# Optimization experiments

Measured on AMD Instinct MI355X. Metric: run time of the kernel, lower is better.

The kernel has to match this reference:

```python
import jax, jax.numpy as jnp
import numpy as np
import math

PHI = (1 + math.sqrt(5)) / 2
PI = math.pi
B, L, D, V, NL, PAD = 2, 384, 256, 32000, 3, 0


def _ln(t, eps):
    mu = t.mean(-1, keepdims=True)
    var = ((t - mu) ** 2).mean(-1, keepdims=True)
    return (t - mu) / jnp.sqrt(var + eps)


def setup_inputs() -> dict:
    key = jax.random.key(0)
    ks = jax.random.split(key, 8)
    return {
        'x': jax.random.randint(ks[0], (B, L), 0, V, dtype=jnp.int32),
        'emb_real': jax.random.normal(ks[1], (V, D), jnp.float32) * 0.02,
        'emb_imag': jax.random.normal(ks[2], (V, D), jnp.float32) * 0.02,
        'layer_phases': jax.random.normal(ks[3], (NL, D), jnp.float32) * 0.02,
        'interference_weights': jax.random.normal(ks[4], (NL, D), jnp.float32) * 0.02,
        'energy_levels': jnp.linspace(0.0, 1.0, D).astype(jnp.float32),
        'excitation_factor': jnp.ones((1,), jnp.float32) * 0.1,
        'phase_preservation': jnp.ones((NL, D), jnp.float32) * 0.1,
        'coherence_factor': jnp.ones((NL, 1), jnp.float32) * 0.1,
        'W_attn': jax.random.normal(ks[5], (NL, D, D), jnp.float32) * 0.02,
        'out_w': jax.random.normal(ks[6], (2 * D, V), jnp.float32) * 0.02,
        'out_b': jnp.zeros((V,), jnp.float32),
    }


def _forward(x, emb_real, emb_imag, layer_phases, interference_weights,
             energy_levels, excitation_factor, phase_preservation,
             coherence_factor, W_attn, out_w, out_b):
    re = emb_real[x] * 0.1                      # [B,L,D]
    _unused_imag = emb_imag[x] * 0.1            # imag embedding unused downstream (as in original)
    # ---- EnhancedDynamicPhaseSpace ----
    fr = jnp.zeros_like(re)
    fi = jnp.zeros_like(re)
    for i in range(NL):
        pa = jnp.tanh(layer_phases[i]) * PI * PHI      # [D]
        r = _ln(re * jnp.cos(pa), 1e-8)
        im = _ln(re * jnp.sin(pa), 1e-8)
        w = jnp.tanh(interference_weights[i])
        r = r * w
        im = im * w
        a = 2.0 * PI * i / NL
        ca, sa = math.cos(a), math.sin(a)
        fr = fr + r * ca - im * sa
        fi = fi + r * sa + im * ca
    amp = jnp.sqrt(fr * fr + fi * fi + 1e-8)
    coll = (amp < 0.1).astype(re.dtype)
    exc = jnp.exp(energy_levels) * excitation_factor   # [D]
    fr = fr + coll * exc
    fi = fi + coll * exc
    nrm = jnp.sqrt(fr * fr + fi * fi + 1e-8)
    real = jnp.clip(fr / nrm, -1.0, 1.0)
    imag = jnp.clip(fi / nrm, -1.0, 1.0)
    # ---- 3 QuantumStatePreservingAttention layers ----
    pad_mask = (x == PAD)                               # [B,L]
    scale = D ** (-0.5)
    for i in range(NL):
        # q/k/v LayerNorms are parameter-free here and q=k=v, so one norm each
        nr = _ln(real, 1e-5)
        ni = _ln(imag, 1e-5)
        ph = jnp.arctan2(ni + 1e-8, nr + 1e-8)          # [B,L,D]
        pdiff = ph[:, :, None, :] - ph[:, None, :, :]   # [B,L,L,D]
        interf = jnp.cos(pdiff)                         # [B,L,L,D]
        # mean over last dim of (interf @ W) == interf . row-means of W (same math)
        w_mean = W_attn[i].mean(axis=1)                 # [D]
        scores = jnp.einsum('blmd,d->blm', interf, w_mean) * scale
        scores = jnp.where(pad_mask[:, None, :], -jnp.inf, scores)
        attn = jnp.clip(jax.nn.softmax(scores, axis=-1), 1e-6, 1.0)
        out_r = jnp.einsum('blm,bmd->bld', attn, nr)
        out_i = jnp.einsum('blm,bmd->bld', attn, ni)
        coh = interf.mean(axis=(-1, -2))                # [B,L]
        cf = jax.nn.sigmoid(coherence_factor[i]) * coh[..., None]
        phase = jnp.arctan2(out_i + 1e-8, out_r + 1e-8)
        pres = jax.nn.sigmoid(phase_preservation[i]) * cf
        pr = out_r * jnp.cos(phase * pres)
        pim = out_i * jnp.sin(phase * pres)
        real = jnp.clip(_ln(real + 0.01 * pr, 1e-8), -1.0, 1.0)
        _dead = _ln(imag + 0.01 * pim, 1e-8)            # computed then overwritten in original
        imag = real                                     # original bug: imag = clamp(real, -1, 1)
    combined = _ln(jnp.concatenate([real, imag], axis=-1), 1e-5)
    logits = jnp.clip((combined @ out_w + out_b) * 0.1, -10.0, 10.0)
    return logits


def reference(x, emb_real, emb_imag, layer_phases, interference_weights,
              energy_levels, excitation_factor, phase_preservation,
              coherence_factor, W_attn, out_w, out_b):
    return _forward(x, emb_real, emb_imag, layer_phases, interference_weights,
                    energy_levels, excitation_factor, phase_preservation,
                    coherence_factor, W_attn, out_w, out_b)
```

## Files before the change

kernel.cpp:

```cpp
#include <hip/hip_runtime.h>
#include <hip/hip_bf16.h>
#include <math.h>

typedef __hip_bfloat16 bf16;
typedef __bf16 bf16x8 __attribute__((ext_vector_type(8)));
typedef float f32x4 __attribute__((ext_vector_type(4)));

#define NTOK 768
#define SEQ  384
#define DDIM 256
#define VOC  32000

__device__ __forceinline__ float bf2f(bf16 v) { return __bfloat162float(v); }

__device__ __forceinline__ bool probe_bf(const void* energy) {
    return ((const unsigned short*)energy)[1] != 0;
}
__device__ __forceinline__ float ldin(const void* p, long i, bool bf) {
    return bf ? bf2f(((const bf16*)p)[i]) : ((const float*)p)[i];
}

__device__ __forceinline__ float blk_sum256(float v, float* red) {
    #pragma unroll
    for (int o = 32; o > 0; o >>= 1) v += __shfl_down(v, o, 64);
    int w = threadIdx.x >> 6;
    __syncthreads();
    if ((threadIdx.x & 63) == 0) red[w] = v;
    __syncthreads();
    return red[0] + red[1] + red[2] + red[3];
}

__global__ __launch_bounds__(256)
void phase_kernel(const int* __restrict__ x, const void* __restrict__ emb,
                  const void* __restrict__ lph, const void* __restrict__ iw,
                  const void* __restrict__ energy, const void* __restrict__ excf,
                  float* __restrict__ realO, float* __restrict__ imagO)
{
    __shared__ float red[4];
    bool bf = probe_bf(energy);
    int t = blockIdx.x, d = threadIdx.x;
    int tok = x[t];
    float re = ldin(emb, (long)tok * DDIM + d, bf) * 0.1f;
    float fr = 0.f, fi = 0.f;
    const float ca[3] = {1.0f, -0.5f, -0.5f};
    const float sa[3] = {0.0f, 0.86602540378443864676f, -0.86602540378443864676f};
    #pragma unroll
    for (int i = 0; i < 3; ++i) {
        float pa = tanhf(ldin(lph, i * DDIM + d, bf)) * 3.14159265358979323846f;
        pa = pa * 1.61803398874989484820f;
        float vr = re * cosf(pa);
        float vi = re * sinf(pa);
        float mu = blk_sum256(vr, red) * (1.f / 256.f);
        float dv = vr - mu;
        float var = blk_sum256(dv * dv, red) * (1.f / 256.f);
        float r = dv / sqrtf(var + 1e-8f);
        mu = blk_sum256(vi, red) * (1.f / 256.f);
        float di = vi - mu;
        var = blk_sum256(di * di, red) * (1.f / 256.f);
        float im = di / sqrtf(var + 1e-8f);
        float w = tanhf(ldin(iw, i * DDIM + d, bf));
        r *= w; im *= w;
        fr = fr + r * ca[i] - im * sa[i];
        fi = fi + r * sa[i] + im * ca[i];
    }
    float amp = sqrtf(fr * fr + fi * fi + 1e-8f);
    float ex = expf(ldin(energy, d, bf)) * ldin(excf, 0, bf);
    if (amp < 0.1f) { fr += ex; fi += ex; }
    float nrm = sqrtf(fr * fr + fi * fi + 1e-8f);
    float rr = fminf(fmaxf(fr / nrm, -1.f), 1.f);
    float ii = fminf(fmaxf(fi / nrm, -1.f), 1.f);
    realO[t * DDIM + d] = rr;
    imagO[t * DDIM + d] = ii;
}

__global__ __launch_bounds__(256)
void wmean_kernel(const void* __restrict__ W, const void* __restrict__ energy,
                  float* __restrict__ wmAll)
{
    bool bf = probe_bf(energy);
    int row = blockIdx.x * 4 + (threadIdx.x >> 6);
    int lane = threadIdx.x & 63;
    long base = (long)row * DDIM + lane * 4;
    float s = 0.f;
    #pragma unroll
    for (int j = 0; j < 4; ++j) s += ldin(W, base + j, bf);
    #pragma unroll
    for (int o = 32; o > 0; o >>= 1) s += __shfl_down(s, o, 64);
    if (lane == 0) wmAll[row] = s * (1.f / 256.f) * 0.0625f;
}

__global__ __launch_bounds__(256)
void normphase_kernel(const float* __restrict__ realI, const float* __restrict__ imagI,
                      const float* __restrict__ wm,
                      float* __restrict__ nrO, float* __restrict__ niO,
                      float* __restrict__ Co, float* __restrict__ So,
                      bf16* __restrict__ ASh, bf16* __restrict__ ASl,
                      bf16* __restrict__ BSh, bf16* __restrict__ BSl)
{
    __shared__ float red[4];
    int t = blockIdx.x, d = threadIdx.x;
    float r = realI[t * DDIM + d];
    float mu = blk_sum256(r, red) * (1.f / 256.f);
    float dv = r - mu;
    float var = blk_sum256(dv * dv, red) * (1.f / 256.f);
    float nr = dv / sqrtf(var + 1e-5f);
    float im = imagI[t * DDIM + d];
    mu = blk_sum256(im, red) * (1.f / 256.f);
    float di = im - mu;
    var = blk_sum256(di * di, red) * (1.f / 256.f);
    float ni = di / sqrtf(var + 1e-5f);
    float ph = atan2f(ni + 1e-8f, nr + 1e-8f);
    float Cv = cosf(ph), Sv = sinf(ph);
    nrO[t * DDIM + d] = nr;
    niO[t * DDIM + d] = ni;
    Co[t * DDIM + d] = Cv;
    So[t * DDIM + d] = Sv;
    float wv = wm[d];
    float aC = Cv * wv, aS = Sv * wv;
    long o0 = (long)t * 512 + d, o1 = o0 + 256;
    bf16 h;
    h = __float2bfloat16(aC); ASh[o0] = h; ASl[o0] = __float2bfloat16(aC - bf2f(h));
    h = __float2bfloat16(aS); ASh[o1] = h; ASl[o1] = __float2bfloat16(aS - bf2f(h));
    h = __float2bfloat16(Cv); BSh[o0] = h; BSl[o0] = __float2bfloat16(Cv - bf2f(h));
    h = __float2bfloat16(Sv); BSh[o1] = h; BSl[o1] = __float2bfloat16(Sv - bf2f(h));
}

__global__ __launch_bounds__(256)
void sums_kernel(const float* __restrict__ C, const float* __restrict__ S,
                 float* __restrict__ Cp, float* __restrict__ Sp)
{
    int c = blockIdx.x, b = blockIdx.y, d = threadIdx.x;
    float cs = 0.f, ss = 0.f;
    int base = (b * SEQ + c * 48) * DDIM + d;
    for (int m = 0; m < 48; ++m) { cs += C[base + m * DDIM]; ss += S[base + m * DDIM]; }
    Cp[(b * 8 + c) * DDIM + d] = cs;
    Sp[(b * 8 + c) * DDIM + d] = ss;
}

__global__ __launch_bounds__(256)
void transpose_kernel(const float* __restrict__ nr, const float* __restrict__ ni,
                      bf16* __restrict__ nrTh, bf16* __restrict__ nrTl,
                      bf16* __restrict__ niTh, bf16* __restrict__ niTl)
{
    __shared__ float tr[64][65], ti[64][65];
    int m0 = blockIdx.x * 64, d0 = blockIdx.y * 64, b = blockIdx.z;
    int c = threadIdx.x & 63, rr = threadIdx.x >> 6;
    #pragma unroll
    for (int i = 0; i < 16; ++i) {
        int r = i * 4 + rr;
        tr[r][c] = nr[(b * SEQ + m0 + r) * DDIM + d0 + c];
        ti[r][c] = ni[(b * SEQ + m0 + r) * DDIM + d0 + c];
    }
    __syncthreads();
    #pragma unroll
    for (int i = 0; i < 16; ++i) {
        int dd = i * 4 + rr;
        float vr = tr[c][dd], vi = ti[c][dd];
        long o = (long)(b * DDIM + d0 + dd) * SEQ + m0 + c;
        bf16 h;
        h = __float2bfloat16(vr); nrTh[o] = h; nrTl[o] = __float2bfloat16(vr - bf2f(h));
        h = __float2bfloat16(vi); niTh[o] = h; niTl[o] = __float2bfloat16(vi - bf2f(h));
    }
}

__device__ __forceinline__ void gload_lds16(const bf16* g, bf16* l) {
    __builtin_amdgcn_global_load_lds(
        (const __attribute__((address_space(1))) unsigned int*)g,
        (__attribute__((address_space(3))) unsigned int*)l,
        16, 0, 0);
}

__global__ __launch_bounds__(256, 2)
void scores_mfma(const bf16* __restrict__ ASh, const bf16* __restrict__ ASl,
                 const bf16* __restrict__ BSh, const bf16* __restrict__ BSl,
                 float* __restrict__ scores)
{
    __shared__ bf16 lds[4][64 * 64];
    int l0 = blockIdx.x * 64, m0 = blockIdx.y * 64, b = blockIdx.z;
    int tid = threadIdx.x, lane = tid & 63, wid = tid >> 6;
    int wr = wid >> 1, wc = wid & 1;

    const bf16* src;
    if      (wid == 0) src = ASh + (size_t)(b * SEQ + l0) * 512;
    else if (wid == 1) src = ASl + (size_t)(b * SEQ + l0) * 512;
    else if (wid == 2) src = BSh + (size_t)(b * SEQ + m0) * 512;
    else               src = BSl + (size_t)(b * SEQ + m0) * 512;
    bf16* ldst = &lds[wid][0];
    int lrow = lane >> 3;
    int cbs  = (lane & 7) ^ lrow;

    f32x4 acc[2][2] = {};

    for (int k0 = 0; k0 < 512; k0 += 64) {
        #pragma unroll
        for (int q = 0; q < 8; ++q) {
            const bf16* g = src + (size_t)(q * 8 + lrow) * 512 + k0 + cbs * 8;
            gload_lds16(g, ldst + q * 512);
        }
        __syncthreads();
        #pragma unroll
        for (int ks = 0; ks < 2; ++ks) {
            int cb = ks * 64 + (lane >> 4) * 16;
            bf16x8 bh[2], bl[2];
            #pragma unroll
            for (int fn = 0; fn < 2; ++fn) {
                int row = wc * 32 + fn * 16 + (lane & 15);
                int off = row * 128 + (cb ^ ((row & 7) << 4));
                bh[fn] = *(const bf16x8*)((const char*)&lds[2][0] + off);
                bl[fn] = *(const bf16x8*)((const char*)&lds[3][0] + off);
            }
            #pragma unroll
            for (int fm = 0; fm < 2; ++fm) {
                int row = wr * 32 + fm * 16 + (lane & 15);
                int off = row * 128 + (cb ^ ((row & 7) << 4));
                bf16x8 ah = *(const bf16x8*)((const char*)&lds[0][0] + off);
                bf16x8 al = *(const bf16x8*)((const char*)&lds[1][0] + off);
                #pragma unroll
                for (int fn = 0; fn < 2; ++fn) {
                    acc[fm][fn] = __builtin_amdgcn_mfma_f32_16x16x32_bf16(ah, bh[fn], acc[fm][fn], 0, 0, 0);
                    acc[fm][fn] = __builtin_amdgcn_mfma_f32_16x16x32_bf16(ah, bl[fn], acc[fm][fn], 0, 0, 0);
                    acc[fm][fn] = __builtin_amdgcn_mfma_f32_16x16x32_bf16(al, bh[fn], acc[fm][fn], 0, 0, 0);
                }
            }
        }
        __syncthreads();
    }

    #pragma unroll
    for (int fn = 0; fn < 2; ++fn) {
        int mm = m0 + wc * 32 + fn * 16 + (lane & 15);
        #pragma unroll
        for (int fm = 0; fm < 2; ++fm) {
            int lbase = l0 + wr * 32 + fm * 16 + (lane >> 4) * 4;
            #pragma unroll
            for (int i = 0; i < 4; ++i)
                scores[(size_t)(b * SEQ + lbase + i) * SEQ + mm] = acc[fm][fn][i];
        }
    }
}

__global__ __launch_bounds__(384)
void softmax_kernel(const float* __restrict__ scores, const int* __restrict__ x,
                    bf16* __restrict__ Ph, bf16* __restrict__ Pl)
{
    __shared__ float red[6];
    int row = blockIdx.x;
    int b = row / SEQ;
    int m = threadIdx.x;
    float s = scores[row * SEQ + m];
    if (x[b * SEQ + m] == 0) s = -__builtin_inff();
    float v = s;
    #pragma unroll
    for (int o = 32; o > 0; o >>= 1) v = fmaxf(v, __shfl_down(v, o, 64));
    if ((threadIdx.x & 63) == 0) red[threadIdx.x >> 6] = v;
    __syncthreads();
    float mx = red[0];
    #pragma unroll
    for (int i = 1; i < 6; ++i) mx = fmaxf(mx, red[i]);
    float p = expf(s - mx);
    __syncthreads();
    v = p;
    #pragma unroll
    for (int o = 32; o > 0; o >>= 1) v += __shfl_down(v, o, 64);
    if ((threadIdx.x & 63) == 0) red[threadIdx.x >> 6] = v;
    __syncthreads();
    float sum = red[0] + red[1] + red[2] + red[3] + red[4] + red[5];
    float pv = p / sum;
    pv = fminf(fmaxf(pv, 1e-6f), 1.0f);
    bf16 h = __float2bfloat16(pv);
    Ph[(size_t)row * SEQ + m] = h;
    Pl[(size_t)row * SEQ + m] = __float2bfloat16(pv - bf2f(h));
}

__global__ __launch_bounds__(256, 4)
void outgemm_mfma(const bf16* __restrict__ Ph, const bf16* __restrict__ Pl,
                  const bf16* __restrict__ nrTh, const bf16* __restrict__ nrTl,
                  const bf16* __restrict__ niTh, const bf16* __restrict__ niTl,
                  float* __restrict__ outr, float* __restrict__ outi)
{
    __shared__ bf16 ldsA[2][64 * 64];
    __shared__ bf16 ldsB[4][32 * 64];
    int l0 = blockIdx.x * 64, d0 = blockIdx.y * 32, b = blockIdx.z;
    int tid = threadIdx.x, lane = tid & 63, wid = tid >> 6;
    int wr = wid >> 1, wc = wid & 1;
    int lrow = lane >> 3, cbs = (lane & 7) ^ lrow;

    const bf16* sA  = (wid == 0 ? Ph : Pl) + (size_t)(b * SEQ + l0) * SEQ;
    const bf16* sB1 = (wid == 2 ? nrTh : nrTl) + (size_t)(b * DDIM + d0) * SEQ;
    const bf16* sB2 = (wid == 2 ? niTh : niTl) + (size_t)(b * DDIM + d0) * SEQ;

    f32x4 accr[2] = {}, acci[2] = {};

    for (int k0 = 0; k0 < SEQ; k0 += 64) {
        if (wid < 2) {
            bf16* ld = &ldsA[wid][0];
            #pragma unroll
            for (int q = 0; q < 8; ++q)
                gload_lds16(sA + (size_t)(q * 8 + lrow) * SEQ + k0 + cbs * 8, ld + q * 512);
        } else {
            bf16* l1 = &ldsB[wid - 2][0];
            bf16* l2 = &ldsB[wid][0];
            #pragma unroll
            for (int q = 0; q < 4; ++q)
                gload_lds16(sB1 + (size_t)(q * 8 + lrow) * SEQ + k0 + cbs * 8, l1 + q * 512);
            #pragma unroll
            for (int q = 0; q < 4; ++q)
                gload_lds16(sB2 + (size_t)(q * 8 + lrow) * SEQ + k0 + cbs * 8, l2 + q * 512);
        }
        __syncthreads();
        #pragma unroll
        for (int ks = 0; ks < 2; ++ks) {
            int cb = ks * 64 + (lane >> 4) * 16;
            int rowb = wc * 16 + (lane & 15);
            int offb = rowb * 128 + (cb ^ ((rowb & 7) << 4));
            bf16x8 brh = *(const bf16x8*)((const char*)&ldsB[0][0] + offb);
            bf16x8 brl = *(const bf16x8*)((const char*)&ldsB[1][0] + offb);
            bf16x8 bih = *(const bf16x8*)((const char*)&ldsB[2][0] + offb);
            bf16x8 bil = *(const bf16x8*)((const char*)&ldsB[3][0] + offb);
            #pragma unroll
            for (int fm = 0; fm < 2; ++fm) {
                int rowa = wr * 32 + fm * 16 + (lane & 15);
                int offa = rowa * 128 + (cb ^ ((rowa & 7) << 4));
                bf16x8 ah = *(const bf16x8*)((const char*)&ldsA[0][0] + offa);
                bf16x8 al = *(const bf16x8*)((const char*)&ldsA[1][0] + offa);
                accr[fm] = __builtin_amdgcn_mfma_f32_16x16x32_bf16(ah, brh, accr[fm], 0, 0, 0);
                accr[fm] = __builtin_amdgcn_mfma_f32_16x16x32_bf16(ah, brl, accr[fm], 0, 0, 0);
                accr[fm] = __builtin_amdgcn_mfma_f32_16x16x32_bf16(al, brh, accr[fm], 0, 0, 0);
                acci[fm] = __builtin_amdgcn_mfma_f32_16x16x32_bf16(ah, bih, acci[fm], 0, 0, 0);
                acci[fm] = __builtin_amdgcn_mfma_f32_16x16x32_bf16(ah, bil, acci[fm], 0, 0, 0);
                acci[fm] = __builtin_amdgcn_mfma_f32_16x16x32_bf16(al, bih, acci[fm], 0, 0, 0);
            }
        }
        __syncthreads();
    }

    int d = d0 + wc * 16 + (lane & 15);
    #pragma unroll
    for (int fm = 0; fm < 2; ++fm) {
        int lb = l0 + wr * 32 + fm * 16 + (lane >> 4) * 4;
        #pragma unroll
        for (int i = 0; i < 4; ++i) {
            size_t idx = (size_t)(b * SEQ + lb + i) * DDIM + d;
            outr[idx] = accr[fm][i];
            outi[idx] = acci[fm][i];
        }
    }
}

__global__ __launch_bounds__(256)
void update_kernel(float* __restrict__ realA, float* __restrict__ imagA,
                   const float* __restrict__ outr, const float* __restrict__ outi,
                   const float* __restrict__ C, const float* __restrict__ S,
                   const float* __restrict__ Cp, const float* __restrict__ Sp,
                   const void* __restrict__ pp, const void* __restrict__ cfac,
                   const void* __restrict__ energy, int layer)
{
    __shared__ float red[4];
    bool bf = probe_bf(energy);
    int t = blockIdx.x, d = threadIdx.x;
    int b = t / SEQ;
    float cs = 0.f, ss = 0.f;
    #pragma unroll
    for (int c = 0; c < 8; ++c) {
        cs += Cp[(b * 8 + c) * DDIM + d];
        ss += Sp[(b * 8 + c) * DDIM + d];
    }
    float dotv = C[t * DDIM + d] * cs + S[t * DDIM + d] * ss;
    float coh = blk_sum256(dotv, red) * (1.0f / (384.f * 256.f));
    float cf = (1.f / (1.f + expf(-ldin(cfac, layer, bf)))) * coh;
    float orr = outr[t * DDIM + d], oii = outi[t * DDIM + d];
    float phase = atan2f(oii + 1e-8f, orr + 1e-8f);
    float pres = (1.f / (1.f + expf(-ldin(pp, layer * DDIM + d, bf)))) * cf;
    float pr = orr * cosf(phase * pres);
    float v = realA[t * DDIM + d] + 0.01f * pr;
    float mu = blk_sum256(v, red) * (1.f / 256.f);
    float dv = v - mu;
    float var = blk_sum256(dv * dv, red) * (1.f / 256.f);
    float nv = dv / sqrtf(var + 1e-8f);
    nv = fminf(fmaxf(nv, -1.f), 1.f);
    realA[t * DDIM + d] = nv;
    imagA[t * DDIM + d] = nv;
}


__global__ __launch_bounds__(256)
void fold_kernel(const void* __restrict__ W, const void* __restrict__ energy,
                 bf16* __restrict__ Bh, bf16* __restrict__ Bl)
{
    __shared__ float tile[64][65];
    bool bf = probe_bf(energy);
    int v0 = blockIdx.x * 64, d0 = blockIdx.y * 64;
    int c = threadIdx.x & 63, rr = threadIdx.x >> 6;
    #pragma unroll
    for (int i = 0; i < 16; ++i) {
        int r = i * 4 + rr;
        long i1 = (long)(d0 + r) * VOC + v0 + c;
        long i2 = (long)(d0 + r + 256) * VOC + v0 + c;
        tile[r][c] = ldin(W, i1, bf) + ldin(W, i2, bf);
    }
    __syncthreads();
    int d = threadIdx.x & 63, vv = threadIdx.x >> 6;
    #pragma unroll
    for (int i = 0; i < 16; ++i) {
        int v = i * 4 + vv;
        float s = tile[d][v];
        bf16 h = __float2bfloat16(s);
        long o = (long)(v0 + v) * DDIM + d0 + d;
        Bh[o] = h;
        Bl[o] = __float2bfloat16(s - __bfloat162float(h));
    }
}

__global__ __launch_bounds__(256)
void prep_kernel(const float* __restrict__ realA, bf16* __restrict__ Ah,
                 bf16* __restrict__ Al)
{
    __shared__ float red[4];
    int t = blockIdx.x, d = threadIdx.x;
    float v = realA[t * DDIM + d];
    float mu = blk_sum256(v, red) * (1.f / 256.f);
    float dv = v - mu;
    float var = blk_sum256(dv * dv, red) * (1.f / 256.f);
    float cval = dv / sqrtf(var + 1e-5f);
    bf16 h = __float2bfloat16(cval);
    Ah[t * DDIM + d] = h;
    Al[t * DDIM + d] = __float2bfloat16(cval - __bfloat162float(h));
}

__global__ __launch_bounds__(512, 4)
void vocab_gemm(const bf16* __restrict__ Ah, const bf16* __restrict__ Al,
                const bf16* __restrict__ Bh, const bf16* __restrict__ Bl,
                const void* __restrict__ bias, const void* __restrict__ energy,
                void* __restrict__ out)
{
    __shared__ bf16 lds[4][128 * 64];
    bool bf = probe_bf(energy);
    int flat = blockIdx.x + blockIdx.y * 6;
    int xcd = flat & 7, bidx = flat >> 3;
    int swz = (xcd < 4) ? xcd * 188 + bidx : 752 + (xcd - 4) * 187 + bidx;
    int m0 = (swz % 6) * 128, n0 = (swz / 6) * 128;
    int tid = threadIdx.x, lane = tid & 63, wid = tid >> 6;
    int wm = wid >> 2, wn = wid & 3;
    int arr = wid >> 1, half = wid & 1;

    const bf16* src;
    if      (arr == 0) src = Ah + (size_t)m0 * DDIM;
    else if (arr == 1) src = Al + (size_t)m0 * DDIM;
    else if (arr == 2) src = Bh + (size_t)n0 * DDIM;
    else               src = Bl + (size_t)n0 * DDIM;
    src += (size_t)half * 64 * DDIM;
    bf16* ldst = &lds[arr][half * 64 * 64];
    int lrow = lane >> 3;
    int cbs  = (lane & 7) ^ lrow;

    f32x4 acc[4][2] = {};

    for (int k0 = 0; k0 < DDIM; k0 += 64) {
        #pragma unroll
        for (int q = 0; q < 8; ++q) {
            const bf16* g = src + (size_t)(q * 8 + lrow) * DDIM + k0 + cbs * 8;
            gload_lds16(g, ldst + q * 512);
        }
        __syncthreads();

        #pragma unroll
        for (int ks = 0; ks < 2; ++ks) {
            int cb = ks * 64 + (lane >> 4) * 16;
            bf16x8 bhf[2], blf[2];
            #pragma unroll
            for (int fn = 0; fn < 2; ++fn) {
                int row = wn * 32 + fn * 16 + (lane & 15);
                int off = row * 128 + (cb ^ ((row & 7) << 4));
                bhf[fn] = *(const bf16x8*)((const char*)&lds[2][0] + off);
                blf[fn] = *(const bf16x8*)((const char*)&lds[3][0] + off);
            }
            #pragma unroll
            for (int fm = 0; fm < 4; ++fm) {
                int row = wm * 64 + fm * 16 + (lane & 15);
                int off = row * 128 + (cb ^ ((row & 7) << 4));
                bf16x8 ah = *(const bf16x8*)((const char*)&lds[0][0] + off);
                bf16x8 al = *(const bf16x8*)((const char*)&lds[1][0] + off);
                #pragma unroll
                for (int fn = 0; fn < 2; ++fn) {
                    acc[fm][fn] = __builtin_amdgcn_mfma_f32_16x16x32_bf16(ah, bhf[fn], acc[fm][fn], 0, 0, 0);
                    acc[fm][fn] = __builtin_amdgcn_mfma_f32_16x16x32_bf16(ah, blf[fn], acc[fm][fn], 0, 0, 0);
                    acc[fm][fn] = __builtin_amdgcn_mfma_f32_16x16x32_bf16(al, bhf[fn], acc[fm][fn], 0, 0, 0);
                }
            }
        }
        __syncthreads();
    }

    #pragma unroll
    for (int fn = 0; fn < 2; ++fn) {
        int n = n0 + wn * 32 + fn * 16 + (lane & 15);
        float bv = ldin(bias, n, bf);
        #pragma unroll
        for (int fm = 0; fm < 4; ++fm) {
            int mbase = m0 + wm * 64 + fm * 16 + (lane >> 4) * 4;
            #pragma unroll
            for (int i = 0; i < 4; ++i) {
                float lg = (acc[fm][fn][i] + bv) * 0.1f;
                lg = fminf(fmaxf(lg, -10.f), 10.f);
                size_t idx = (size_t)(mbase + i) * VOC + n;
                if (bf) ((bf16*)out)[idx] = __float2bfloat16(lg);
                else    ((float*)out)[idx] = lg;
            }
        }
    }
}

extern "C" void kernel_launch(void* const* d_in, const int* in_sizes, int n_in,
                              void* d_out, int out_size, void* d_ws, size_t ws_size,
                              hipStream_t stream) {
    (void)in_sizes; (void)n_in; (void)out_size; (void)ws_size;
    const int*  x        = (const int*)d_in[0];
    const void* emb_real = d_in[1];
    const void* lph      = d_in[3];
    const void* iw       = d_in[4];
    const void* energy   = d_in[5];
    const void* excf     = d_in[6];
    const void* pp       = d_in[7];
    const void* cfac     = d_in[8];
    const void* Wattn    = d_in[9];
    const void* out_w    = d_in[10];
    const void* out_b    = d_in[11];

    float* ws = (float*)d_ws;
    const int TD = NTOK * DDIM;
    float* realA = ws;
    float* imagA = realA + TD;
    float* nr    = imagA + TD;
    float* ni    = nr + TD;
    float* Cc    = ni + TD;
    float* Ss    = Cc + TD;
    float* outr  = Ss + TD;
    float* outi  = outr + TD;
    float* attn  = outi + TD;
    float* Cp    = attn + 2 * SEQ * SEQ;
    float* Sp    = Cp + 16 * DDIM;
    bf16* Ah  = (bf16*)(Sp + 16 * DDIM);
    bf16* Al  = Ah + (size_t)NTOK * DDIM;
    bf16* Wth = Al + (size_t)NTOK * DDIM;
    bf16* Wtl = Wth + (size_t)VOC * DDIM;
    bf16* ASh = Wtl + (size_t)VOC * DDIM;
    bf16* ASl = ASh + (size_t)NTOK * 512;
    bf16* BSh = ASl + (size_t)NTOK * 512;
    bf16* BSl = BSh + (size_t)NTOK * 512;
    bf16* Phb = BSl + (size_t)NTOK * 512;
    bf16* Plb = Phb + (size_t)NTOK * SEQ;
    bf16* nrTh = Plb + (size_t)NTOK * SEQ;
    bf16* nrTl = nrTh + (size_t)NTOK * DDIM;
    bf16* niTh = nrTl + (size_t)NTOK * DDIM;
    bf16* niTl = niTh + (size_t)NTOK * DDIM;
    float* wmAll = (float*)(niTl + (size_t)NTOK * DDIM);

    fold_kernel<<<dim3(VOC / 64, DDIM / 64), 256, 0, stream>>>(out_w, energy, Wth, Wtl);
    wmean_kernel<<<192, 256, 0, stream>>>(Wattn, energy, wmAll);

    phase_kernel<<<NTOK, 256, 0, stream>>>(x, emb_real, lph, iw, energy, excf, realA, imagA);
    for (int layer = 0; layer < 3; ++layer) {
        normphase_kernel<<<NTOK, 256, 0, stream>>>(realA, imagA, wmAll + layer * DDIM,
                                                   nr, ni, Cc, Ss, ASh, ASl, BSh, BSl);
        sums_kernel<<<dim3(8, 2), 256, 0, stream>>>(Cc, Ss, Cp, Sp);
        transpose_kernel<<<dim3(6, 4, 2), 256, 0, stream>>>(nr, ni, nrTh, nrTl, niTh, niTl);
        scores_mfma<<<dim3(6, 6, 2), 256, 0, stream>>>(ASh, ASl, BSh, BSl, attn);
        softmax_kernel<<<NTOK, 384, 0, stream>>>(attn, x, Phb, Plb);
        outgemm_mfma<<<dim3(6, 8, 2), 256, 0, stream>>>(Phb, Plb, nrTh, nrTl, niTh, niTl, outr, outi);
        update_kernel<<<NTOK, 256, 0, stream>>>(realA, imagA, outr, outi, Cc, Ss, Cp, Sp,
                                                pp, cfac, energy, layer);
    }
    prep_kernel<<<NTOK, 256, 0, stream>>>(realA, Ah, Al);
    vocab_gemm<<<dim3(6, VOC / 128), 512, 0, stream>>>(Ah, Al, Wth, Wtl, out_b, energy, (void*)d_out);
}
```

Before: 384.6 us.

## Fuse layernorm-phase prep into neighbors and skip redundant imaginary path after layer zero

Removes normphase_kernel and prep_kernel by folding their layernorm and phase/cos/sin/bf16-split output into the end of phase_kernel and update_kernel. It also uses the fact that imag equals real after the first layer, so the imaginary transpose, GEMM and stores are skipped for later layers. The scores GEMM tile is narrowed to 64x32 to launch more blocks, and the column-sum kernel is split into more chunks. This cuts kernel launches and duplicate memory traffic, at the cost of more reductions and more register use inside the fused kernels.

```diff
diff --git a/kernel.cpp b/kernel.cpp
--- a/kernel.cpp
+++ b/kernel.cpp
@@ -30,11 +30,40 @@
     return red[0] + red[1] + red[2] + red[3];
 }
 
+__device__ __forceinline__ void np_emit(int t, int d, float nrv, float niv, bool dual,
+                                        const float* __restrict__ wm,
+                                        float* __restrict__ nrO, float* __restrict__ niO,
+                                        float* __restrict__ Co, float* __restrict__ So,
+                                        bf16* __restrict__ ASh, bf16* __restrict__ ASl,
+                                        bf16* __restrict__ BSh, bf16* __restrict__ BSl)
+{
+    float ph = atan2f(niv + 1e-8f, nrv + 1e-8f);
+    float Cv = cosf(ph), Sv = sinf(ph);
+    long idx = (long)t * DDIM + d;
+    nrO[idx] = nrv;
+    if (dual) niO[idx] = niv;
+    Co[idx] = Cv;
+    So[idx] = Sv;
+    float wv = wm[d];
+    float aC = Cv * wv, aS = Sv * wv;
+    long o0 = (long)t * 512 + d, o1 = o0 + 256;
+    bf16 h;
+    h = __float2bfloat16(aC); ASh[o0] = h; ASl[o0] = __float2bfloat16(aC - bf2f(h));
+    h = __float2bfloat16(aS); ASh[o1] = h; ASl[o1] = __float2bfloat16(aS - bf2f(h));
+    h = __float2bfloat16(Cv); BSh[o0] = h; BSl[o0] = __float2bfloat16(Cv - bf2f(h));
+    h = __float2bfloat16(Sv); BSh[o1] = h; BSl[o1] = __float2bfloat16(Sv - bf2f(h));
+}
+
 __global__ __launch_bounds__(256)
 void phase_kernel(const int* __restrict__ x, const void* __restrict__ emb,
                   const void* __restrict__ lph, const void* __restrict__ iw,
                   const void* __restrict__ energy, const void* __restrict__ excf,
-                  float* __restrict__ realO, float* __restrict__ imagO)
+                  const float* __restrict__ wm0,
+                  float* __restrict__ realO,
+                  float* __restrict__ nrO, float* __restrict__ niO,
+                  float* __restrict__ Co, float* __restrict__ So,
+                  bf16* __restrict__ ASh, bf16* __restrict__ ASl,
+                  bf16* __restrict__ BSh, bf16* __restrict__ BSl)
 {
     __shared__ float red[4];
     bool bf = probe_bf(energy);
@@ -70,7 +99,15 @@
     float rr = fminf(fmaxf(fr / nrm, -1.f), 1.f);
     float ii = fminf(fmaxf(fi / nrm, -1.f), 1.f);
     realO[t * DDIM + d] = rr;
-    imagO[t * DDIM + d] = ii;
+    float mu = blk_sum256(rr, red) * (1.f / 256.f);
+    float dv = rr - mu;
+    float var = blk_sum256(dv * dv, red) * (1.f / 256.f);
+    float nrv = dv / sqrtf(var + 1e-5f);
+    mu = blk_sum256(ii, red) * (1.f / 256.f);
+    float di = ii - mu;
+    var = blk_sum256(di * di, red) * (1.f / 256.f);
+    float niv = di / sqrtf(var + 1e-5f);
+    np_emit(t, d, nrv, niv, true, wm0, nrO, niO, Co, So, ASh, ASl, BSh, BSl);
 }
 
 __global__ __launch_bounds__(256)
@@ -90,57 +127,22 @@
 }
 
 __global__ __launch_bounds__(256)
-void normphase_kernel(const float* __restrict__ realI, const float* __restrict__ imagI,
-                      const float* __restrict__ wm,
-                      float* __restrict__ nrO, float* __restrict__ niO,
-                      float* __restrict__ Co, float* __restrict__ So,
-                      bf16* __restrict__ ASh, bf16* __restrict__ ASl,
-                      bf16* __restrict__ BSh, bf16* __restrict__ BSl)
-{
-    __shared__ float red[4];
-    int t = blockIdx.x, d = threadIdx.x;
-    float r = realI[t * DDIM + d];
-    float mu = blk_sum256(r, red) * (1.f / 256.f);
-    float dv = r - mu;
-    float var = blk_sum256(dv * dv, red) * (1.f / 256.f);
-    float nr = dv / sqrtf(var + 1e-5f);
-    float im = imagI[t * DDIM + d];
-    mu = blk_sum256(im, red) * (1.f / 256.f);
-    float di = im - mu;
-    var = blk_sum256(di * di, red) * (1.f / 256.f);
-    float ni = di / sqrtf(var + 1e-5f);
-    float ph = atan2f(ni + 1e-8f, nr + 1e-8f);
-    float Cv = cosf(ph), Sv = sinf(ph);
-    nrO[t * DDIM + d] = nr;
-    niO[t * DDIM + d] = ni;
-    Co[t * DDIM + d] = Cv;
-    So[t * DDIM + d] = Sv;
-    float wv = wm[d];
-    float aC = Cv * wv, aS = Sv * wv;
-    long o0 = (long)t * 512 + d, o1 = o0 + 256;
-    bf16 h;
-    h = __float2bfloat16(aC); ASh[o0] = h; ASl[o0] = __float2bfloat16(aC - bf2f(h));
-    h = __float2bfloat16(aS); ASh[o1] = h; ASl[o1] = __float2bfloat16(aS - bf2f(h));
-    h = __float2bfloat16(Cv); BSh[o0] = h; BSl[o0] = __float2bfloat16(Cv - bf2f(h));
-    h = __float2bfloat16(Sv); BSh[o1] = h; BSl[o1] = __float2bfloat16(Sv - bf2f(h));
-}
-
-__global__ __launch_bounds__(256)
 void sums_kernel(const float* __restrict__ C, const float* __restrict__ S,
                  float* __restrict__ Cp, float* __restrict__ Sp)
 {
     int c = blockIdx.x, b = blockIdx.y, d = threadIdx.x;
     float cs = 0.f, ss = 0.f;
-    int base = (b * SEQ + c * 48) * DDIM + d;
-    for (int m = 0; m < 48; ++m) { cs += C[base + m * DDIM]; ss += S[base + m * DDIM]; }
-    Cp[(b * 8 + c) * DDIM + d] = cs;
-    Sp[(b * 8 + c) * DDIM + d] = ss;
+    int base = (b * SEQ + c * 16) * DDIM + d;
+    #pragma unroll
+    for (int m = 0; m < 16; ++m) { cs += C[base + m * DDIM]; ss += S[base + m * DDIM]; }
+    Cp[(b * 24 + c) * DDIM + d] = cs;
+    Sp[(b * 24 + c) * DDIM + d] = ss;
 }
 
 __global__ __launch_bounds__(256)
 void transpose_kernel(const float* __restrict__ nr, const float* __restrict__ ni,
                       bf16* __restrict__ nrTh, bf16* __restrict__ nrTl,
-                      bf16* __restrict__ niTh, bf16* __restrict__ niTl)
+                      bf16* __restrict__ niTh, bf16* __restrict__ niTl, int dual)
 {
     __shared__ float tr[64][65], ti[64][65];
     int m0 = blockIdx.x * 64, d0 = blockIdx.y * 64, b = blockIdx.z;
@@ -149,17 +151,20 @@
     for (int i = 0; i < 16; ++i) {
         int r = i * 4 + rr;
         tr[r][c] = nr[(b * SEQ + m0 + r) * DDIM + d0 + c];
-        ti[r][c] = ni[(b * SEQ + m0 + r) * DDIM + d0 + c];
+        if (dual) ti[r][c] = ni[(b * SEQ + m0 + r) * DDIM + d0 + c];
     }
     __syncthreads();
     #pragma unroll
     for (int i = 0; i < 16; ++i) {
         int dd = i * 4 + rr;
-        float vr = tr[c][dd], vi = ti[c][dd];
         long o = (long)(b * DDIM + d0 + dd) * SEQ + m0 + c;
+        float vr = tr[c][dd];
         bf16 h;
         h = __float2bfloat16(vr); nrTh[o] = h; nrTl[o] = __float2bfloat16(vr - bf2f(h));
-        h = __float2bfloat16(vi); niTh[o] = h; niTl[o] = __float2bfloat16(vi - bf2f(h));
+        if (dual) {
+            float vi = ti[c][dd];
+            h = __float2bfloat16(vi); niTh[o] = h; niTl[o] = __float2bfloat16(vi - bf2f(h));
+        }
     }
 }
 
@@ -170,72 +175,65 @@
         16, 0, 0);
 }
 
-__global__ __launch_bounds__(256, 2)
+__global__ __launch_bounds__(256, 4)
 void scores_mfma(const bf16* __restrict__ ASh, const bf16* __restrict__ ASl,
                  const bf16* __restrict__ BSh, const bf16* __restrict__ BSl,
                  float* __restrict__ scores)
 {
-    __shared__ bf16 lds[4][64 * 64];
-    int l0 = blockIdx.x * 64, m0 = blockIdx.y * 64, b = blockIdx.z;
+    __shared__ bf16 ldsA[2][64 * 64];
+    __shared__ bf16 ldsB[2][32 * 64];
+    int l0 = blockIdx.x * 64, m0 = blockIdx.y * 32, b = blockIdx.z;
     int tid = threadIdx.x, lane = tid & 63, wid = tid >> 6;
     int wr = wid >> 1, wc = wid & 1;
-
-    const bf16* src;
-    if      (wid == 0) src = ASh + (size_t)(b * SEQ + l0) * 512;
-    else if (wid == 1) src = ASl + (size_t)(b * SEQ + l0) * 512;
-    else if (wid == 2) src = BSh + (size_t)(b * SEQ + m0) * 512;
-    else               src = BSl + (size_t)(b * SEQ + m0) * 512;
-    bf16* ldst = &lds[wid][0];
     int lrow = lane >> 3;
     int cbs  = (lane & 7) ^ lrow;
 
-    f32x4 acc[2][2] = {};
+    const bf16* srcA = (wid == 1 ? ASl : ASh) + (size_t)(b * SEQ + l0) * 512;
+    const bf16* srcB = (wid == 3 ? BSl : BSh) + (size_t)(b * SEQ + m0) * 512;
+
+    f32x4 acc[2] = {};
 
     for (int k0 = 0; k0 < 512; k0 += 64) {
-        #pragma unroll
-        for (int q = 0; q < 8; ++q) {
-            const bf16* g = src + (size_t)(q * 8 + lrow) * 512 + k0 + cbs * 8;
-            gload_lds16(g, ldst + q * 512);
+        if (wid < 2) {
+            bf16* ld = &ldsA[wid][0];
+            #pragma unroll
+            for (int q = 0; q < 8; ++q)
+                gload_lds16(srcA + (size_t)(q * 8 + lrow) * 512 + k0 + cbs * 8, ld + q * 512);
+        } else {
+            bf16* ld = &ldsB[wid - 2][0];
+            #pragma unroll
+            for (int q = 0; q < 4; ++q)
+                gload_lds16(srcB + (size_t)(q * 8 + lrow) * 512 + k0 + cbs * 8, ld + q * 512);
         }
         __syncthreads();
         #pragma unroll
         for (int ks = 0; ks < 2; ++ks) {
             int cb = ks * 64 + (lane >> 4) * 16;
-            bf16x8 bh[2], bl[2];
-            #pragma unroll
-            for (int fn = 0; fn < 2; ++fn) {
-                int row = wc * 32 + fn * 16 + (lane & 15);
-                int off = row * 128 + (cb ^ ((row & 7) << 4));
-                bh[fn] = *(const bf16x8*)((const char*)&lds[2][0] + off);
-                bl[fn] = *(const bf16x8*)((const char*)&lds[3][0] + off);
-            }
+            int rowb = wc * 16 + (lane & 15);
+            int offb = rowb * 128 + (cb ^ ((rowb & 7) << 4));
+            bf16x8 bh = *(const bf16x8*)((const char*)&ldsB[0][0] + offb);
+            bf16x8 bl = *(const bf16x8*)((const char*)&ldsB[1][0] + offb);
             #pragma unroll
             for (int fm = 0; fm < 2; ++fm) {
-                int row = wr * 32 + fm * 16 + (lane & 15);
-                int off = row * 128 + (cb ^ ((row & 7) << 4));
-                bf16x8 ah = *(const bf16x8*)((const char*)&lds[0][0] + off);
-                bf16x8 al = *(const bf16x8*)((const char*)&lds[1][0] + off);
-                #pragma unroll
-                for (int fn = 0; fn < 2; ++fn) {
-                    acc[fm][fn] = __builtin_amdgcn_mfma_f32_16x16x32_bf16(ah, bh[fn], acc[fm][fn], 0, 0, 0);
-                    acc[fm][fn] = __builtin_amdgcn_mfma_f32_16x16x32_bf16(ah, bl[fn], acc[fm][fn], 0, 0, 0);
-                    acc[fm][fn] = __builtin_amdgcn_mfma_f32_16x16x32_bf16(al, bh[fn], acc[fm][fn], 0, 0, 0);
-                }
+                int rowa = wr * 32 + fm * 16 + (lane & 15);
+                int offa = rowa * 128 + (cb ^ ((rowa & 7) << 4));
+                bf16x8 ah = *(const bf16x8*)((const char*)&ldsA[0][0] + offa);
+                bf16x8 al = *(const bf16x8*)((const char*)&ldsA[1][0] + offa);
+                acc[fm] = __builtin_amdgcn_mfma_f32_16x16x32_bf16(ah, bh, acc[fm], 0, 0, 0);
+                acc[fm] = __builtin_amdgcn_mfma_f32_16x16x32_bf16(ah, bl, acc[fm], 0, 0, 0);
+                acc[fm] = __builtin_amdgcn_mfma_f32_16x16x32_bf16(al, bh, acc[fm], 0, 0, 0);
             }
         }
         __syncthreads();
     }
 
-    #pragma unroll
-    for (int fn = 0; fn < 2; ++fn) {
-        int mm = m0 + wc * 32 + fn * 16 + (lane & 15);
-        #pragma unroll
-        for (int fm = 0; fm < 2; ++fm) {
-            int lbase = l0 + wr * 32 + fm * 16 + (lane >> 4) * 4;
-            #pragma unroll
-            for (int i = 0; i < 4; ++i)
-                scores[(size_t)(b * SEQ + lbase + i) * SEQ + mm] = acc[fm][fn][i];
-        }
+    int mm = m0 + wc * 16 + (lane & 15);
+    #pragma unroll
+    for (int fm = 0; fm < 2; ++fm) {
+        int lbase = l0 + wr * 32 + fm * 16 + (lane >> 4) * 4;
+        #pragma unroll
+        for (int i = 0; i < 4; ++i)
+            scores[(size_t)(b * SEQ + lbase + i) * SEQ + mm] = acc[fm][i];
     }
 }
 
@@ -276,7 +274,7 @@
 void outgemm_mfma(const bf16* __restrict__ Ph, const bf16* __restrict__ Pl,
                   const bf16* __restrict__ nrTh, const bf16* __restrict__ nrTl,
                   const bf16* __restrict__ niTh, const bf16* __restrict__ niTl,
-                  float* __restrict__ outr, float* __restrict__ outi)
+                  float* __restrict__ outr, float* __restrict__ outi, int dual)
 {
     __shared__ bf16 ldsA[2][64 * 64];
     __shared__ bf16 ldsB[4][32 * 64];
@@ -299,13 +297,15 @@
                 gload_lds16(sA + (size_t)(q * 8 + lrow) * SEQ + k0 + cbs * 8, ld + q * 512);
         } else {
             bf16* l1 = &ldsB[wid - 2][0];
-            bf16* l2 = &ldsB[wid][0];
             #pragma unroll
             for (int q = 0; q < 4; ++q)
                 gload_lds16(sB1 + (size_t)(q * 8 + lrow) * SEQ + k0 + cbs * 8, l1 + q * 512);
-            #pragma unroll
-            for (int q = 0; q < 4; ++q)
-                gload_lds16(sB2 + (size_t)(q * 8 + lrow) * SEQ + k0 + cbs * 8, l2 + q * 512);
+            if (dual) {
+                bf16* l2 = &ldsB[wid][0];
+                #pragma unroll
+                for (int q = 0; q < 4; ++q)
+                    gload_lds16(sB2 + (size_t)(q * 8 + lrow) * SEQ + k0 + cbs * 8, l2 + q * 512);
+            }
         }
         __syncthreads();
         #pragma unroll
@@ -315,8 +315,6 @@
             int offb = rowb * 128 + (cb ^ ((rowb & 7) << 4));
             bf16x8 brh = *(const bf16x8*)((const char*)&ldsB[0][0] + offb);
             bf16x8 brl = *(const bf16x8*)((const char*)&ldsB[1][0] + offb);
-            bf16x8 bih = *(const bf16x8*)((const char*)&ldsB[2][0] + offb);
-            bf16x8 bil = *(const bf16x8*)((const char*)&ldsB[3][0] + offb);
             #pragma unroll
             for (int fm = 0; fm < 2; ++fm) {
                 int rowa = wr * 32 + fm * 16 + (lane & 15);
@@ -326,9 +324,20 @@
                 accr[fm] = __builtin_amdgcn_mfma_f32_16x16x32_bf16(ah, brh, accr[fm], 0, 0, 0);
                 accr[fm] = __builtin_amdgcn_mfma_f32_16x16x32_bf16(ah, brl, accr[fm], 0, 0, 0);
                 accr[fm] = __builtin_amdgcn_mfma_f32_16x16x32_bf16(al, brh, accr[fm], 0, 0, 0);
-                acci[fm] = __builtin_amdgcn_mfma_f32_16x16x32_bf16(ah, bih, acci[fm], 0, 0, 0);
-                acci[fm] = __builtin_amdgcn_mfma_f32_16x16x32_bf16(ah, bil, acci[fm], 0, 0, 0);
-                acci[fm] = __builtin_amdgcn_mfma_f32_16x16x32_bf16(al, bih, acci[fm], 0, 0, 0);
+            }
+            if (dual) {
+                bf16x8 bih = *(const bf16x8*)((const char*)&ldsB[2][0] + offb);
+                bf16x8 bil = *(const bf16x8*)((const char*)&ldsB[3][0] + offb);
+                #pragma unroll
+                for (int fm = 0; fm < 2; ++fm) {
+                    int rowa = wr * 32 + fm * 16 + (lane & 15);
+                    int offa = rowa * 128 + (cb ^ ((rowa & 7) << 4));
+                    bf16x8 ah = *(const bf16x8*)((const char*)&ldsA[0][0] + offa);
+                    bf16x8 al = *(const bf16x8*)((const char*)&ldsA[1][0] + offa);
+                    acci[fm] = __builtin_amdgcn_mfma_f32_16x16x32_bf16(ah, bih, acci[fm], 0, 0, 0);
+                    acci[fm] = __builtin_amdgcn_mfma_f32_16x16x32_bf16(ah, bil, acci[fm], 0, 0, 0);
+                    acci[fm] = __builtin_amdgcn_mfma_f32_16x16x32_bf16(al, bih, acci[fm], 0, 0, 0);
+                }
             }
         }
         __syncthreads();
@@ -342,44 +351,60 @@
         for (int i = 0; i < 4; ++i) {
             size_t idx = (size_t)(b * SEQ + lb + i) * DDIM + d;
             outr[idx] = accr[fm][i];
-            outi[idx] = acci[fm][i];
+            if (dual) outi[idx] = acci[fm][i];
         }
     }
 }
 
 __global__ __launch_bounds__(256)
-void update_kernel(float* __restrict__ realA, float* __restrict__ imagA,
+void update_kernel(float* __restrict__ realA,
                    const float* __restrict__ outr, const float* __restrict__ outi,
                    const float* __restrict__ C, const float* __restrict__ S,
                    const float* __restrict__ Cp, const float* __restrict__ Sp,
                    const void* __restrict__ pp, const void* __restrict__ cfac,
-                   const void* __restrict__ energy, int layer)
+                   const void* __restrict__ energy, int layer, int mode,
+                   const float* __restrict__ wmNext,
+                   float* __restrict__ nrO, float* __restrict__ Co, float* __restrict__ So,
+                   bf16* __restrict__ ASh, bf16* __restrict__ ASl,
+                   bf16* __restrict__ BSh, bf16* __restrict__ BSl,
+                   bf16* __restrict__ Ah, bf16* __restrict__ Al)
 {
     __shared__ float red[4];
     bool bf = probe_bf(energy);
     int t = blockIdx.x, d = threadIdx.x;
     int b = t / SEQ;
+    long idx = (long)t * DDIM + d;
     float cs = 0.f, ss = 0.f;
     #pragma unroll
-    for (int c = 0; c < 8; ++c) {
-        cs += Cp[(b * 8 + c) * DDIM + d];
-        ss += Sp[(b * 8 + c) * DDIM + d];
-    }
-    float dotv = C[t * DDIM + d] * cs + S[t * DDIM + d] * ss;
+    for (int c = 0; c < 24; ++c) {
+        cs += Cp[(b * 24 + c) * DDIM + d];
+        ss += Sp[(b * 24 + c) * DDIM + d];
+    }
+    float dotv = C[idx] * cs + S[idx] * ss;
     float coh = blk_sum256(dotv, red) * (1.0f / (384.f * 256.f));
     float cf = (1.f / (1.f + expf(-ldin(cfac, layer, bf)))) * coh;
-    float orr = outr[t * DDIM + d], oii = outi[t * DDIM + d];
+    float orr = outr[idx], oii = outi[idx];
     float phase = atan2f(oii + 1e-8f, orr + 1e-8f);
     float pres = (1.f / (1.f + expf(-ldin(pp, layer * DDIM + d, bf)))) * cf;
     float pr = orr * cosf(phase * pres);
-    float v = realA[t * DDIM + d] + 0.01f * pr;
+    float v = realA[idx] + 0.01f * pr;
     float mu = blk_sum256(v, red) * (1.f / 256.f);
     float dv = v - mu;
     float var = blk_sum256(dv * dv, red) * (1.f / 256.f);
     float nv = dv / sqrtf(var + 1e-8f);
     nv = fminf(fmaxf(nv, -1.f), 1.f);
-    realA[t * DDIM + d] = nv;
-    imagA[t * DDIM + d] = nv;
+    realA[idx] = nv;
+    float mu2 = blk_sum256(nv, red) * (1.f / 256.f);
+    float dv2 = nv - mu2;
+    float var2 = blk_sum256(dv2 * dv2, red) * (1.f / 256.f);
+    float nn = dv2 / sqrtf(var2 + 1e-5f);
+    if (mode == 0) {
+        np_emit(t, d, nn, nn, false, wmNext, nrO, nullptr, Co, So, ASh, ASl, BSh, BSl);
+    } else {
+        bf16 h = __float2bfloat16(nn);
+        Ah[idx] = h;
+        Al[idx] = __float2bfloat16(nn - bf2f(h));
+    }
 }
 
 
@@ -409,22 +434,6 @@
         Bh[o] = h;
         Bl[o] = __float2bfloat16(s - __bfloat162float(h));
     }
-}
-
-__global__ __launch_bounds__(256)
-void prep_kernel(const float* __restrict__ realA, bf16* __restrict__ Ah,
-                 bf16* __restrict__ Al)
-{
-    __shared__ float red[4];
-    int t = blockIdx.x, d = threadIdx.x;
-    float v = realA[t * DDIM + d];
-    float mu = blk_sum256(v, red) * (1.f / 256.f);
-    float dv = v - mu;
-    float var = blk_sum256(dv * dv, red) * (1.f / 256.f);
-    float cval = dv / sqrtf(var + 1e-5f);
-    bf16 h = __float2bfloat16(cval);
-    Ah[t * DDIM + d] = h;
-    Al[t * DDIM + d] = __float2bfloat16(cval - __bfloat162float(h));
 }
 
 __global__ __launch_bounds__(512, 4)
@@ -529,8 +538,7 @@
     float* ws = (float*)d_ws;
     const int TD = NTOK * DDIM;
     float* realA = ws;
-    float* imagA = realA + TD;
-    float* nr    = imagA + TD;
+    float* nr    = realA + TD;
     float* ni    = nr + TD;
     float* Cc    = ni + TD;
     float* Ss    = Cc + TD;
@@ -538,8 +546,9 @@
     float* outi  = outr + TD;
     float* attn  = outi + TD;
     float* Cp    = attn + 2 * SEQ * SEQ;
-    float* Sp    = Cp + 16 * DDIM;
-    bf16* Ah  = (bf16*)(Sp + 16 * DDIM);
+    float* Sp    = Cp + 48 * DDIM;
+    float* wmAll = Sp + 48 * DDIM;
+    bf16* Ah  = (bf16*)(wmAll + 768);
     bf16* Al  = Ah + (size_t)NTOK * DDIM;
     bf16* Wth = Al + (size_t)NTOK * DDIM;
     bf16* Wtl = Wth + (size_t)VOC * DDIM;
@@ -553,23 +562,25 @@
     bf16* nrTl = nrTh + (size_t)NTOK * DDIM;
     bf16* niTh = nrTl + (size_t)NTOK * DDIM;
     bf16* niTl = niTh + (size_t)NTOK * DDIM;
-    float* wmAll = (float*)(niTl + (size_t)NTOK * DDIM);
 
     fold_kernel<<<dim3(VOC / 64, DDIM / 64), 256, 0, stream>>>(out_w, energy, Wth, Wtl);
     wmean_kernel<<<192, 256, 0, stream>>>(Wattn, energy, wmAll);
 
-    phase_kernel<<<NTOK, 256, 0, stream>>>(x, emb_real, lph, iw, energy, excf, realA, imagA);
+    phase_kernel<<<NTOK, 256, 0, stream>>>(x, emb_real, lph, iw, energy, excf, wmAll,
+                                           realA, nr, ni, Cc, Ss, ASh, ASl, BSh, BSl);
     for (int layer = 0; layer < 3; ++layer) {
-        normphase_kernel<<<NTOK, 256, 0, stream>>>(realA, imagA, wmAll + layer * DDIM,
-                                                   nr, ni, Cc, Ss, ASh, ASl, BSh, BSl);
-        sums_kernel<<<dim3(8, 2), 256, 0, stream>>>(Cc, Ss, Cp, Sp);
-        transpose_kernel<<<dim3(6, 4, 2), 256, 0, stream>>>(nr, ni, nrTh, nrTl, niTh, niTl);
-        scores_mfma<<<dim3(6, 6, 2), 256, 0, stream>>>(ASh, ASl, BSh, BSl, attn);
+        int dual = (layer == 0);
+        sums_kernel<<<dim3(24, 2), 256, 0, stream>>>(Cc, Ss, Cp, Sp);
+        transpose_kernel<<<dim3(6, 4, 2), 256, 0, stream>>>(nr, ni, nrTh, nrTl, niTh, niTl, dual);
+        scores_mfma<<<dim3(6, 12, 2), 256, 0, stream>>>(ASh, ASl, BSh, BSl, attn);
         softmax_kernel<<<NTOK, 384, 0, stream>>>(attn, x, Phb, Plb);
-        outgemm_mfma<<<dim3(6, 8, 2), 256, 0, stream>>>(Phb, Plb, nrTh, nrTl, niTh, niTl, outr, outi);
-        update_kernel<<<NTOK, 256, 0, stream>>>(realA, imagA, outr, outi, Cc, Ss, Cp, Sp,
-                                                pp, cfac, energy, layer);
-    }
-    prep_kernel<<<NTOK, 256, 0, stream>>>(realA, Ah, Al);
+        outgemm_mfma<<<dim3(6, 8, 2), 256, 0, stream>>>(Phb, Plb, nrTh, nrTl, niTh, niTl,
+                                                        outr, outi, dual);
+        update_kernel<<<NTOK, 256, 0, stream>>>(realA, outr, dual ? outi : outr, Cc, Ss,
+                                                Cp, Sp, pp, cfac, energy, layer,
+                                                (layer < 2) ? 0 : 1,
+                                                wmAll + (layer + 1 < 3 ? (layer + 1) * DDIM : 0),
+                                                nr, Cc, Ss, ASh, ASl, BSh, BSl, Ah, Al);
+    }
     vocab_gemm<<<dim3(6, VOC / 128), 512, 0, stream>>>(Ah, Al, Wth, Wtl, out_b, energy, (void*)d_out);
 }
```

Result: faster. 367.7 us (-4.4%).
